# Performance work log

Hardware: AMD Instinct MI355X
Metric: run time of the kernel (lower is better)

The kernel has to match this reference:

```python
import jax, jax.numpy as jnp
import numpy as np

EPS = 1e-5


def _bn(x, g, b, m, v):
    # eval-mode BatchNorm over the last (channel) axis
    return g * (x - m) * jax.lax.rsqrt(v + EPS) + b


def setup_inputs() -> dict:
    key = jax.random.key(0)
    ks = jax.random.split(key, 16)
    B, N, K, C, Cout, G = 2, 16384, 32, 64, 64, 10
    inp = {
        "points": jax.random.normal(ks[0], (B, N, 3), jnp.float32),
        "features": jax.random.normal(ks[1], (B, N, C), jnp.float32),
        "grouped_idx": jax.random.randint(ks[2], (B, N, K), 0, N, jnp.int32),
        # pos_proj: Conv2d(geo_ch, in_ch, 1) + BN + ReLU
        "W_pos": jax.random.normal(ks[3], (C, G), jnp.float32) / np.sqrt(G),
        "b_pos": jnp.zeros((C,), jnp.float32),
        "bn1_g": jnp.ones((C,), jnp.float32),
        "bn1_b": jnp.zeros((C,), jnp.float32),
        "bn1_m": jax.random.normal(ks[4], (C,), jnp.float32) * 0.1,
        "bn1_v": jax.random.uniform(ks[5], (C,), jnp.float32, 0.5, 1.5),
        # gcm_layer: Conv2d(in_ch, in_ch, 1) + BN + ReLU
        "W_gcm": jax.random.normal(ks[6], (C, C), jnp.float32) / np.sqrt(C),
        "b_gcm": jnp.zeros((C,), jnp.float32),
        "bn2_g": jnp.ones((C,), jnp.float32),
        "bn2_b": jnp.zeros((C,), jnp.float32),
        "bn2_m": jax.random.normal(ks[7], (C,), jnp.float32) * 0.1,
        "bn2_v": jax.random.uniform(ks[8], (C,), jnp.float32, 0.5, 1.5),
        # att_conv_catfea: Linear(nsample, 1)
        "W_att": jax.random.normal(ks[9], (K,), jnp.float32) / np.sqrt(K),
        "b_att": jnp.zeros((), jnp.float32),
        # out_layer: Linear(in_ch, out_ch) + LayerNorm + ReLU
        "W_out": jax.random.normal(ks[10], (Cout, C), jnp.float32) / np.sqrt(C),
        "b_out": jnp.zeros((Cout,), jnp.float32),
        "ln_g": jnp.ones((Cout,), jnp.float32),
        "ln_b": jnp.zeros((Cout,), jnp.float32),
    }
    return inp


def reference(points, features, grouped_idx, W_pos, b_pos, bn1_g, bn1_b, bn1_m, bn1_v,
              W_gcm, b_gcm, bn2_g, bn2_b, bn2_m, bn2_v, W_att, b_att,
              W_out, b_out, ln_g, ln_b):
    gather = jax.vmap(lambda arr, idx: arr[idx])  # [N,C],[N,K] -> [N,K,C]
    grouped_points = gather(points, grouped_idx)          # [B,N,K,3]
    grouped_f = gather(features, grouped_idx)             # [B,N,K,C]

    # legacy geometric encoding: [xi, xj, xi - xj, ||xi - xj||] -> geo_ch = 10
    xi = points[:, :, None, :]
    diff = xi - grouped_points
    dist = jnp.linalg.norm(diff, axis=-1, keepdims=True)
    geo = jnp.concatenate(
        [jnp.broadcast_to(xi, grouped_points.shape), grouped_points, diff, dist], axis=-1)

    # pos_proj: 1x1 conv == channel linear, + BN + ReLU
    expanded = jax.nn.relu(_bn(jnp.einsum('bnkg,cg->bnkc', geo, W_pos) + b_pos,
                               bn1_g, bn1_b, bn1_m, bn1_v))

    h = grouped_f + expanded
    # gcm_layer
    h = jax.nn.relu(_bn(jnp.einsum('bnkc,dc->bnkd', h, W_gcm) + b_gcm,
                        bn2_g, bn2_b, bn2_m, bn2_v))

    # attention over neighbor dim K -> score per channel, softmax over channels (dim=2 of [B,N,C,1])
    score = jnp.einsum('bnkc,k->bnc', h, W_att) + b_att   # [B,N,C]
    score = jax.nn.softmax(score, axis=-1)
    h = h * score[:, :, None, :]                          # [B,N,K,C]

    pooled = jnp.max(h, axis=2)                           # maxpooling downsample -> [B,N,C]
    res = pooled + features

    # out_layer: Linear + LayerNorm + ReLU
    y = jnp.einsum('bnc,oc->bno', res, W_out) + b_out
    mu = jnp.mean(y, axis=-1, keepdims=True)
    var = jnp.var(y, axis=-1, keepdims=True)
    y = ln_g * (y - mu) * jax.lax.rsqrt(var + EPS) + ln_b
    return jax.nn.relu(y)
```

## Files before the change

### kernel.cpp

```cpp
#include <hip/hip_runtime.h>
#include <hip/hip_bf16.h>

#define EPSF 1e-5f

typedef __attribute__((ext_vector_type(8))) short bf16x8;
typedef __attribute__((ext_vector_type(4))) float f32x4;
typedef __attribute__((ext_vector_type(2))) unsigned int u32x2;
typedef __attribute__((ext_vector_type(4))) unsigned int u32x4;
typedef __attribute__((ext_vector_type(4))) int i32x4;

constexpr int B_ = 2, N_ = 16384;
constexpr int HSTR = 72;
constexpr int RSTR = 72;
constexpr int PPW  = 4;
constexpr int PPB  = 16;
constexpr size_t PP_BYTES = (size_t)B_ * N_ * 16;

__device__ __forceinline__ short f2bf(float f) {
    __hip_bfloat16 h = __float2bfloat16(f);
    short s; __builtin_memcpy(&s, &h, 2); return s;
}
__device__ __forceinline__ unsigned int pkbf(float a, float b) {
    float2 f2; f2.x = a; f2.y = b;
    __hip_bfloat162 h = __float22bfloat162_rn(f2);
    unsigned int u; __builtin_memcpy(&u, &h, 4); return u;
}

__global__ __launch_bounds__(256) void prep_points(
    const float* __restrict__ pts, float* __restrict__ pp)
{
    const int i = blockIdx.x * 256 + threadIdx.x;
    if (i < B_ * N_) {
        f32x4 o = { pts[3 * i], pts[3 * i + 1], pts[3 * i + 2], 0.f };
        ((f32x4*)pp)[i] = o;
    }
}

template<bool PAD>
__global__ __launch_bounds__(256) void bridgenet8(
    const float* __restrict__ points,
    const float* __restrict__ pp,
    const float* __restrict__ features,
    const int*   __restrict__ gidx,
    const float* __restrict__ Wpos,
    const float* __restrict__ bposv,
    const float* __restrict__ bn1g, const float* __restrict__ bn1b,
    const float* __restrict__ bn1m, const float* __restrict__ bn1v,
    const float* __restrict__ Wgcm,
    const float* __restrict__ bgcm,
    const float* __restrict__ bn2g, const float* __restrict__ bn2b,
    const float* __restrict__ bn2m, const float* __restrict__ bn2v,
    const float* __restrict__ Watt,
    const float* __restrict__ batt,
    const float* __restrict__ Wout,
    const float* __restrict__ bout,
    const float* __restrict__ lng, const float* __restrict__ lnb,
    float* __restrict__ out)
{
    __shared__ __align__(16) short hbuf[4][32 * HSTR];
    __shared__ __align__(16) short resstage[PPB * RSTR];
    __shared__ __align__(16) short wb2[8 * 64 * 8];
    __shared__ __align__(16) short wb3[8 * 64 * 8];

    const int t    = threadIdx.x;
    const int w    = t >> 6;
    const int l    = t & 63;
    const int l15  = l & 15;
    const int quad = l >> 4;
    const int c4   = l15 * 4;

    const int wg  = blockIdx.x;
    const int blk = ((wg & 7) >> 2) * 1024 + (wg >> 3) * 4 + (wg & 3);

    {
        #pragma unroll
        for (int u = 0; u < 4; ++u) {
            const int s  = w * 4 + u;
            const int nt = (s >> 1) & 3, ks = s & 1;
            const float* src = (s < 8 ? Wgcm : Wout) + (c4 + nt) * 64 + ks * 32 + quad * 8;
            const f32x4 w0 = *(const f32x4*)src;
            const f32x4 w1 = *(const f32x4*)(src + 4);
            bf16x8 f;
            #pragma unroll
            for (int j = 0; j < 4; ++j) {
                f[j]     = f2bf(w0[j]);
                f[j + 4] = f2bf(w1[j]);
            }
            short* dst = (s < 8 ? wb2 : wb3);
            *(bf16x8*)&dst[((s & 7) * 64 + l) * 8] = f;
        }
    }

    bf16x8 bposf[4];
    #pragma unroll
    for (int nt = 0; nt < 4; ++nt) {
        const int c = c4 + nt;
        #pragma unroll
        for (int j = 0; j < 8; ++j) {
            const int g = quad * 8 + j;
            bposf[nt][j] = f2bf(g < 10 ? Wpos[c * 10 + g] : 0.f);
        }
    }
    f32x4 ps1, pb1, ps2, pb2;
    {
        const f32x4 g1 = *(const f32x4*)(bn1g + c4);
        const f32x4 b1 = *(const f32x4*)(bn1b + c4);
        const f32x4 m1 = *(const f32x4*)(bn1m + c4);
        const f32x4 v1 = *(const f32x4*)(bn1v + c4);
        const f32x4 bp = *(const f32x4*)(bposv + c4);
        const f32x4 g2 = *(const f32x4*)(bn2g + c4);
        const f32x4 b2 = *(const f32x4*)(bn2b + c4);
        const f32x4 m2 = *(const f32x4*)(bn2m + c4);
        const f32x4 v2 = *(const f32x4*)(bn2v + c4);
        const f32x4 bg = *(const f32x4*)(bgcm + c4);
        #pragma unroll
        for (int j = 0; j < 4; ++j) {
            ps1[j] = g1[j] * rsqrtf(v1[j] + EPSF);
            pb1[j] = ps1[j] * (bp[j] - m1[j]) + b1[j];
            ps2[j] = g2[j] * rsqrtf(v2[j] + EPSF);
            pb2[j] = ps2[j] * (bg[j] - m2[j]) + b2[j];
        }
    }
    float wat[2][4];
    #pragma unroll
    for (int mt = 0; mt < 2; ++mt)
        #pragma unroll
        for (int r = 0; r < 4; ++r)
            wat[mt][r] = Watt[mt * 16 + quad * 4 + r];
    const float battv = batt[0];

    const f32x4 zero4 = {0.f, 0.f, 0.f, 0.f};
    short* hb = hbuf[w];
    const int base = blk * PPB + w * PPW;
    const int bb   = (blk >> 10) * N_;

    auto LOADI = [&](int pt, i32x4 (&gi)[2]) {
        gi[0] = *(const i32x4*)(gidx + (size_t)pt * 32 + quad * 4);
        gi[1] = *(const i32x4*)(gidx + (size_t)pt * 32 + 16 + quad * 4);
    };
    auto LOADD = [&](int pt, const i32x4 (&gi)[2],
                     f32x4 (&f4)[2][4], bf16x8 (&ageo)[2]) {
        #pragma unroll
        for (int mt = 0; mt < 2; ++mt)
            #pragma unroll
            for (int r = 0; r < 4; ++r)
                f4[mt][r] = *(const f32x4*)(features + (size_t)(bb + gi[mt][r]) * 64 + c4);
        int gv[2];
        gv[0] = gidx[(size_t)pt * 32 + l15];
        gv[1] = gidx[(size_t)pt * 32 + 16 + l15];
        float xi0, xi1, xi2, px[2], py[2], pz[2];
        if (PAD) {
            const f32x4 x4 = *(const f32x4*)(pp + (size_t)pt * 4);
            xi0 = x4[0]; xi1 = x4[1]; xi2 = x4[2];
            #pragma unroll
            for (int mt = 0; mt < 2; ++mt) {
                const f32x4 p4 = *(const f32x4*)(pp + (size_t)(bb + gv[mt]) * 4);
                px[mt] = p4[0]; py[mt] = p4[1]; pz[mt] = p4[2];
            }
        } else {
            xi0 = points[(size_t)pt * 3];
            xi1 = points[(size_t)pt * 3 + 1];
            xi2 = points[(size_t)pt * 3 + 2];
            #pragma unroll
            for (int mt = 0; mt < 2; ++mt) {
                const float* ppt = points + (size_t)(bb + gv[mt]) * 3;
                px[mt] = ppt[0]; py[mt] = ppt[1]; pz[mt] = ppt[2];
            }
        }
        #pragma unroll
        for (int mt = 0; mt < 2; ++mt) {
            const float dx = xi0 - px[mt], dy = xi1 - py[mt], dz = xi2 - pz[mt];
            const float dist = sqrtf(dx * dx + dy * dy + dz * dz);
            u32x4 u = {0u, 0u, 0u, 0u};
            if (quad == 0) {
                u[0] = pkbf(xi0, xi1); u[1] = pkbf(xi2, px[mt]);
                u[2] = pkbf(py[mt], pz[mt]); u[3] = pkbf(dx, dy);
            } else if (quad == 1) {
                u[0] = pkbf(dz, dist);
            }
            __builtin_memcpy(&ageo[mt], &u, 16);
        }
    };

    i32x4 giC[2], giN[2];
    LOADI(base, giC);
    LOADI(base + 1, giN);
    f32x4  f4c[2][4];
    bf16x8 ageoc[2];
    LOADD(base, giC, f4c, ageoc);

    __syncthreads();

    #pragma unroll
    for (int i = 0; i < PPW; ++i) {
        const int pt = base + i;

        f32x4  f4n[2][4];
        bf16x8 ageon[2];
        i32x4  giN2[2];
        if (i + 1 < PPW) LOADD(pt + 1, giN, f4n, ageon);
        if (i + 2 < PPW) LOADI(pt + 2, giN2);

        const f32x4 resid = *(const f32x4*)(features + (size_t)pt * 64 + c4);

        f32x4 acc1[2][4];
        #pragma unroll
        for (int mt = 0; mt < 2; ++mt)
            #pragma unroll
            for (int nt = 0; nt < 4; ++nt)
                acc1[mt][nt] = __builtin_amdgcn_mfma_f32_16x16x32_bf16(
                    ageoc[mt], bposf[nt], zero4, 0, 0, 0);

        #pragma unroll
        for (int mt = 0; mt < 2; ++mt)
            #pragma unroll
            for (int r = 0; r < 4; ++r) {
                const int k = mt * 16 + quad * 4 + r;
                float v[4];
                #pragma unroll
                for (int j = 0; j < 4; ++j)
                    v[j] = f4c[mt][r][j] + fmaxf(ps1[j] * acc1[mt][j][r] + pb1[j], 0.f);
                u32x2 hv = { pkbf(v[0], v[1]), pkbf(v[2], v[3]) };
                *(u32x2*)&hb[k * HSTR + c4] = hv;
            }

        bf16x8 a2[2][2];
        #pragma unroll
        for (int mt = 0; mt < 2; ++mt)
            #pragma unroll
            for (int ks = 0; ks < 2; ++ks)
                a2[mt][ks] = *(const bf16x8*)&hb[(mt * 16 + l15) * HSTR + ks * 32 + quad * 8];
        f32x4 acc2[2][4];
        #pragma unroll
        for (int nt = 0; nt < 4; ++nt) {
            const bf16x8 b0 = *(const bf16x8*)&wb2[((nt * 2 + 0) * 64 + l) * 8];
            const bf16x8 b1 = *(const bf16x8*)&wb2[((nt * 2 + 1) * 64 + l) * 8];
            #pragma unroll
            for (int mt = 0; mt < 2; ++mt) {
                f32x4 a = __builtin_amdgcn_mfma_f32_16x16x32_bf16(a2[mt][0], b0, zero4, 0, 0, 0);
                acc2[mt][nt] = __builtin_amdgcn_mfma_f32_16x16x32_bf16(a2[mt][1], b1, a, 0, 0, 0);
            }
        }

        float res[4];
        {
            float sp[4], mk[4];
            #pragma unroll
            for (int nt = 0; nt < 4; ++nt) {
                sp[nt] = 0.f; mk[nt] = 0.f;
                #pragma unroll
                for (int mt = 0; mt < 2; ++mt)
                    #pragma unroll
                    for (int r = 0; r < 4; ++r) {
                        const float h2 = fmaxf(ps2[nt] * acc2[mt][nt][r] + pb2[nt], 0.f);
                        sp[nt] += h2 * wat[mt][r];
                        mk[nt] = fmaxf(mk[nt], h2);
                    }
                sp[nt] += __shfl_xor(sp[nt], 16);
                sp[nt] += __shfl_xor(sp[nt], 32);
                mk[nt] = fmaxf(mk[nt], __shfl_xor(mk[nt], 16));
                mk[nt] = fmaxf(mk[nt], __shfl_xor(mk[nt], 32));
            }
            float e[4], s = 0.f;
            #pragma unroll
            for (int nt = 0; nt < 4; ++nt) { e[nt] = __expf(sp[nt] + battv); s += e[nt]; }
            #pragma unroll
            for (int o = 1; o < 16; o <<= 1) s += __shfl_xor(s, o);
            const float inv = 1.f / s;
            #pragma unroll
            for (int nt = 0; nt < 4; ++nt)
                res[nt] = e[nt] * inv * mk[nt] + resid[nt];
        }
        if (quad == 0) {
            u32x2 rv = { pkbf(res[0], res[1]), pkbf(res[2], res[3]) };
            *(u32x2*)&resstage[(w * PPW + i) * RSTR + c4] = rv;
        }

        if (i + 1 < PPW) {
            #pragma unroll
            for (int mt = 0; mt < 2; ++mt) {
                #pragma unroll
                for (int r = 0; r < 4; ++r) f4c[mt][r] = f4n[mt][r];
                ageoc[mt] = ageon[mt];
            }
            if (i + 2 < PPW) { giN[0] = giN2[0]; giN[1] = giN2[1]; }
        }
    }

    __syncthreads();

    const f32x4 lngv  = *(const f32x4*)(lng + c4);
    const f32x4 lnbv  = *(const f32x4*)(lnb + c4);
    const f32x4 boutv = *(const f32x4*)(bout + c4);
    bf16x8 a3[2];
    #pragma unroll
    for (int ks = 0; ks < 2; ++ks)
        a3[ks] = *(const bf16x8*)&resstage[l15 * RSTR + ks * 32 + quad * 8];
    f32x4 acc3[4];
    #pragma unroll
    for (int nt = 0; nt < 4; ++nt) {
        const bf16x8 b0 = *(const bf16x8*)&wb3[((nt * 2 + 0) * 64 + l) * 8];
        const bf16x8 b1 = *(const bf16x8*)&wb3[((nt * 2 + 1) * 64 + l) * 8];
        f32x4 a = __builtin_amdgcn_mfma_f32_16x16x32_bf16(a3[0], b0, zero4, 0, 0, 0);
        acc3[nt] = __builtin_amdgcn_mfma_f32_16x16x32_bf16(a3[1], b1, a, 0, 0, 0);
    }
    float y[4], s = 0.f;
    #pragma unroll
    for (int nt = 0; nt < 4; ++nt) { y[nt] = acc3[nt][w] + boutv[nt]; s += y[nt]; }
    #pragma unroll
    for (int o = 1; o < 16; o <<= 1) s += __shfl_xor(s, o);
    const float mu = s * (1.f / 64.f);
    float dv[4], v2 = 0.f;
    #pragma unroll
    for (int nt = 0; nt < 4; ++nt) { dv[nt] = y[nt] - mu; v2 += dv[nt] * dv[nt]; }
    #pragma unroll
    for (int o = 1; o < 16; o <<= 1) v2 += __shfl_xor(v2, o);
    const float rs = rsqrtf(v2 * (1.f / 64.f) + EPSF);
    const int pto = blk * PPB + quad * 4 + w;
    f32x4 ov;
    #pragma unroll
    for (int nt = 0; nt < 4; ++nt)
        ov[nt] = fmaxf(lngv[nt] * dv[nt] * rs + lnbv[nt], 0.f);
    *(f32x4*)(out + (size_t)pto * 64 + c4) = ov;
}

extern "C" void kernel_launch(void* const* d_in, const int* in_sizes, int n_in,
                              void* d_out, int out_size, void* d_ws, size_t ws_size,
                              hipStream_t stream) {
    const float* points   = (const float*)d_in[0];
    const float* features = (const float*)d_in[1];
    const int*   gidxp    = (const int*)d_in[2];
    const bool   pad      = (ws_size >= PP_BYTES);
    float* pp = (float*)d_ws;
    if (pad) {
        hipLaunchKernelGGL(prep_points, dim3((B_ * N_ + 255) / 256), dim3(256), 0, stream,
                           points, pp);
        hipLaunchKernelGGL((bridgenet8<true>), dim3((B_ * N_) / PPB), dim3(256), 0, stream,
            points, pp, features, gidxp,
            (const float*)d_in[3],  (const float*)d_in[4],
            (const float*)d_in[5],  (const float*)d_in[6],  (const float*)d_in[7],  (const float*)d_in[8],
            (const float*)d_in[9],  (const float*)d_in[10],
            (const float*)d_in[11], (const float*)d_in[12], (const float*)d_in[13], (const float*)d_in[14],
            (const float*)d_in[15], (const float*)d_in[16],
            (const float*)d_in[17], (const float*)d_in[18],
            (const float*)d_in[19], (const float*)d_in[20],
            (float*)d_out);
    } else {
        hipLaunchKernelGGL((bridgenet8<false>), dim3((B_ * N_) / PPB), dim3(256), 0, stream,
            points, pp, features, gidxp,
            (const float*)d_in[3],  (const float*)d_in[4],
            (const float*)d_in[5],  (const float*)d_in[6],  (const float*)d_in[7],  (const float*)d_in[8],
            (const float*)d_in[9],  (const float*)d_in[10],
            (const float*)d_in[11], (const float*)d_in[12], (const float*)d_in[13], (const float*)d_in[14],
            (const float*)d_in[15], (const float*)d_in[16],
            (const float*)d_in[17], (const float*)d_in[18],
            (const float*)d_in[19], (const float*)d_in[20],
            (float*)d_out);
    }
}
```

Before: 180.6 us.

## Use 8 waves per block with 2 points each, add MFMA priority hints

Each block now runs 512 threads (8 waves), each wave handling 2 points instead of 4, so more waves are in flight to hide gather latency. Launch bounds ask for 4 blocks per CU. The residual feature load moves into the prefetch routine, the two-ahead index prefetch is dropped, and s_setprio raises wave priority around the MFMA sections. The output stage is limited to the first 4 waves. The cost is less per-wave software pipelining, more LDS per block, and idle waves during the final stage.

After: 267.3 us. 48.0% more time.

```diff
diff --git a/kernel.cpp b/kernel.cpp
--- a/kernel.cpp
+++ b/kernel.cpp
@@ -12,7 +12,8 @@
 constexpr int B_ = 2, N_ = 16384;
 constexpr int HSTR = 72;
 constexpr int RSTR = 72;
-constexpr int PPW  = 4;
+constexpr int PPW  = 2;
+constexpr int NW   = 8;
 constexpr int PPB  = 16;
 constexpr size_t PP_BYTES = (size_t)B_ * N_ * 16;
 
@@ -37,7 +38,7 @@
 }
 
 template<bool PAD>
-__global__ __launch_bounds__(256) void bridgenet8(
+__global__ __launch_bounds__(512, 4) void bridgenet9(
     const float* __restrict__ points,
     const float* __restrict__ pp,
     const float* __restrict__ features,
@@ -57,7 +58,7 @@
     const float* __restrict__ lng, const float* __restrict__ lnb,
     float* __restrict__ out)
 {
-    __shared__ __align__(16) short hbuf[4][32 * HSTR];
+    __shared__ __align__(16) short hbuf[NW][32 * HSTR];
     __shared__ __align__(16) short resstage[PPB * RSTR];
     __shared__ __align__(16) short wb2[8 * 64 * 8];
     __shared__ __align__(16) short wb3[8 * 64 * 8];
@@ -74,8 +75,8 @@
 
     {
         #pragma unroll
-        for (int u = 0; u < 4; ++u) {
-            const int s  = w * 4 + u;
+        for (int u = 0; u < 2; ++u) {
+            const int s  = w * 2 + u;
             const int nt = (s >> 1) & 3, ks = s & 1;
             const float* src = (s < 8 ? Wgcm : Wout) + (c4 + nt) * 64 + ks * 32 + quad * 8;
             const f32x4 w0 = *(const f32x4*)src;
@@ -139,12 +140,13 @@
         gi[1] = *(const i32x4*)(gidx + (size_t)pt * 32 + 16 + quad * 4);
     };
     auto LOADD = [&](int pt, const i32x4 (&gi)[2],
-                     f32x4 (&f4)[2][4], bf16x8 (&ageo)[2]) {
+                     f32x4 (&f4)[2][4], bf16x8 (&ageo)[2], f32x4& resid) {
         #pragma unroll
         for (int mt = 0; mt < 2; ++mt)
             #pragma unroll
             for (int r = 0; r < 4; ++r)
                 f4[mt][r] = *(const f32x4*)(features + (size_t)(bb + gi[mt][r]) * 64 + c4);
+        resid = *(const f32x4*)(features + (size_t)pt * 64 + c4);
         int gv[2];
         gv[0] = gidx[(size_t)pt * 32 + l15];
         gv[1] = gidx[(size_t)pt * 32 + 16 + l15];
@@ -187,22 +189,22 @@
     LOADI(base + 1, giN);
     f32x4  f4c[2][4];
     bf16x8 ageoc[2];
-    LOADD(base, giC, f4c, ageoc);
+    f32x4  residc;
+    LOADD(base, giC, f4c, ageoc, residc);
 
     __syncthreads();
 
     #pragma unroll
     for (int i = 0; i < PPW; ++i) {
         const int pt = base + i;
+        (void)pt;
 
         f32x4  f4n[2][4];
         bf16x8 ageon[2];
-        i32x4  giN2[2];
-        if (i + 1 < PPW) LOADD(pt + 1, giN, f4n, ageon);
-        if (i + 2 < PPW) LOADI(pt + 2, giN2);
-
-        const f32x4 resid = *(const f32x4*)(features + (size_t)pt * 64 + c4);
-
+        f32x4  residn;
+        if (i + 1 < PPW) LOADD(base + i + 1, giN, f4n, ageon, residn);
+
+        __builtin_amdgcn_s_setprio(1);
         f32x4 acc1[2][4];
         #pragma unroll
         for (int mt = 0; mt < 2; ++mt)
@@ -210,6 +212,7 @@
             for (int nt = 0; nt < 4; ++nt)
                 acc1[mt][nt] = __builtin_amdgcn_mfma_f32_16x16x32_bf16(
                     ageoc[mt], bposf[nt], zero4, 0, 0, 0);
+        __builtin_amdgcn_s_setprio(0);
 
         #pragma unroll
         for (int mt = 0; mt < 2; ++mt)
@@ -230,6 +233,7 @@
             #pragma unroll
             for (int ks = 0; ks < 2; ++ks)
                 a2[mt][ks] = *(const bf16x8*)&hb[(mt * 16 + l15) * HSTR + ks * 32 + quad * 8];
+        __builtin_amdgcn_s_setprio(1);
         f32x4 acc2[2][4];
         #pragma unroll
         for (int nt = 0; nt < 4; ++nt) {
@@ -241,6 +245,7 @@
                 acc2[mt][nt] = __builtin_amdgcn_mfma_f32_16x16x32_bf16(a2[mt][1], b1, a, 0, 0, 0);
             }
         }
+        __builtin_amdgcn_s_setprio(0);
 
         float res[4];
         {
@@ -269,7 +274,7 @@
             const float inv = 1.f / s;
             #pragma unroll
             for (int nt = 0; nt < 4; ++nt)
-                res[nt] = e[nt] * inv * mk[nt] + resid[nt];
+                res[nt] = e[nt] * inv * mk[nt] + residc[nt];
         }
         if (quad == 0) {
             u32x2 rv = { pkbf(res[0], res[1]), pkbf(res[2], res[3]) };
@@ -283,45 +288,47 @@
                 for (int r = 0; r < 4; ++r) f4c[mt][r] = f4n[mt][r];
                 ageoc[mt] = ageon[mt];
             }
-            if (i + 2 < PPW) { giN[0] = giN2[0]; giN[1] = giN2[1]; }
+            residc = residn;
         }
     }
 
     __syncthreads();
 
-    const f32x4 lngv  = *(const f32x4*)(lng + c4);
-    const f32x4 lnbv  = *(const f32x4*)(lnb + c4);
-    const f32x4 boutv = *(const f32x4*)(bout + c4);
-    bf16x8 a3[2];
-    #pragma unroll
-    for (int ks = 0; ks < 2; ++ks)
-        a3[ks] = *(const bf16x8*)&resstage[l15 * RSTR + ks * 32 + quad * 8];
-    f32x4 acc3[4];
-    #pragma unroll
-    for (int nt = 0; nt < 4; ++nt) {
-        const bf16x8 b0 = *(const bf16x8*)&wb3[((nt * 2 + 0) * 64 + l) * 8];
-        const bf16x8 b1 = *(const bf16x8*)&wb3[((nt * 2 + 1) * 64 + l) * 8];
-        f32x4 a = __builtin_amdgcn_mfma_f32_16x16x32_bf16(a3[0], b0, zero4, 0, 0, 0);
-        acc3[nt] = __builtin_amdgcn_mfma_f32_16x16x32_bf16(a3[1], b1, a, 0, 0, 0);
-    }
-    float y[4], s = 0.f;
-    #pragma unroll
-    for (int nt = 0; nt < 4; ++nt) { y[nt] = acc3[nt][w] + boutv[nt]; s += y[nt]; }
-    #pragma unroll
-    for (int o = 1; o < 16; o <<= 1) s += __shfl_xor(s, o);
-    const float mu = s * (1.f / 64.f);
-    float dv[4], v2 = 0.f;
-    #pragma unroll
-    for (int nt = 0; nt < 4; ++nt) { dv[nt] = y[nt] - mu; v2 += dv[nt] * dv[nt]; }
-    #pragma unroll
-    for (int o = 1; o < 16; o <<= 1) v2 += __shfl_xor(v2, o);
-    const float rs = rsqrtf(v2 * (1.f / 64.f) + EPSF);
-    const int pto = blk * PPB + quad * 4 + w;
-    f32x4 ov;
-    #pragma unroll
-    for (int nt = 0; nt < 4; ++nt)
-        ov[nt] = fmaxf(lngv[nt] * dv[nt] * rs + lnbv[nt], 0.f);
-    *(f32x4*)(out + (size_t)pto * 64 + c4) = ov;
+    if (w < 4) {
+        const f32x4 lngv  = *(const f32x4*)(lng + c4);
+        const f32x4 lnbv  = *(const f32x4*)(lnb + c4);
+        const f32x4 boutv = *(const f32x4*)(bout + c4);
+        bf16x8 a3[2];
+        #pragma unroll
+        for (int ks = 0; ks < 2; ++ks)
+            a3[ks] = *(const bf16x8*)&resstage[l15 * RSTR + ks * 32 + quad * 8];
+        f32x4 acc3[4];
+        #pragma unroll
+        for (int nt = 0; nt < 4; ++nt) {
+            const bf16x8 b0 = *(const bf16x8*)&wb3[((nt * 2 + 0) * 64 + l) * 8];
+            const bf16x8 b1 = *(const bf16x8*)&wb3[((nt * 2 + 1) * 64 + l) * 8];
+            f32x4 a = __builtin_amdgcn_mfma_f32_16x16x32_bf16(a3[0], b0, zero4, 0, 0, 0);
+            acc3[nt] = __builtin_amdgcn_mfma_f32_16x16x32_bf16(a3[1], b1, a, 0, 0, 0);
+        }
+        float y[4], s = 0.f;
+        #pragma unroll
+        for (int nt = 0; nt < 4; ++nt) { y[nt] = acc3[nt][w] + boutv[nt]; s += y[nt]; }
+        #pragma unroll
+        for (int o = 1; o < 16; o <<= 1) s += __shfl_xor(s, o);
+        const float mu = s * (1.f / 64.f);
+        float dv[4], v2 = 0.f;
+        #pragma unroll
+        for (int nt = 0; nt < 4; ++nt) { dv[nt] = y[nt] - mu; v2 += dv[nt] * dv[nt]; }
+        #pragma unroll
+        for (int o = 1; o < 16; o <<= 1) v2 += __shfl_xor(v2, o);
+        const float rs = rsqrtf(v2 * (1.f / 64.f) + EPSF);
+        const int pto = blk * PPB + quad * 4 + w;
+        f32x4 ov;
+        #pragma unroll
+        for (int nt = 0; nt < 4; ++nt)
+            ov[nt] = fmaxf(lngv[nt] * dv[nt] * rs + lnbv[nt], 0.f);
+        *(f32x4*)(out + (size_t)pto * 64 + c4) = ov;
+    }
 }
 
 extern "C" void kernel_launch(void* const* d_in, const int* in_sizes, int n_in,
@@ -335,7 +342,7 @@
     if (pad) {
         hipLaunchKernelGGL(prep_points, dim3((B_ * N_ + 255) / 256), dim3(256), 0, stream,
                            points, pp);
-        hipLaunchKernelGGL((bridgenet8<true>), dim3((B_ * N_) / PPB), dim3(256), 0, stream,
+        hipLaunchKernelGGL((bridgenet9<true>), dim3((B_ * N_) / PPB), dim3(512), 0, stream,
             points, pp, features, gidxp,
             (const float*)d_in[3],  (const float*)d_in[4],
             (const float*)d_in[5],  (const float*)d_in[6],  (const float*)d_in[7],  (const float*)d_in[8],
@@ -346,7 +353,7 @@
             (const float*)d_in[19], (const float*)d_in[20],
             (float*)d_out);
     } else {
-        hipLaunchKernelGGL((bridgenet8<false>), dim3((B_ * N_) / PPB), dim3(256), 0, stream,
+        hipLaunchKernelGGL((bridgenet9<false>), dim3((B_ * N_) / PPB), dim3(512), 0, stream,
             points, pp, features, gidxp,
             (const float*)d_in[3],  (const float*)d_in[4],
             (const float*)d_in[5],  (const float*)d_in[6],  (const float*)d_in[7],  (const float*)d_in[8],
```
